# Performance work log

Hardware: AMD Instinct MI355X
Metric: run time of the kernel (lower is better)

The kernel has to match this reference:

```python
import jax, jax.numpy as jnp
import numpy as np

H, KV, D, HID = 36, 4, 128, 4608   # heads, kv heads, head_dim, hidden
THETA = 100000.0
NEG = -1e30


def _rope_neox(pos, x):
    # pos: [T] int, x: [T, nh, D]; neox style: rotate half
    half = D // 2
    inv_freq = 1.0 / (THETA ** (jnp.arange(half, dtype=jnp.float32) / half))
    ang = pos.astype(jnp.float32)[:, None] * inv_freq          # [T, half]
    cos = jnp.cos(ang)[:, None, :]
    sin = jnp.sin(ang)[:, None, :]
    x1, x2 = x[..., :half], x[..., half:]
    return jnp.concatenate([x1 * cos - x2 * sin, x2 * cos + x1 * sin], axis=-1)


def setup_inputs() -> dict:
    key = jax.random.key(0)
    ks = jax.random.split(key, 6)
    T = 2048
    return {
        "positions": jnp.arange(T, dtype=jnp.int32),
        "hidden_states": jax.random.normal(ks[0], (T, HID), dtype=jnp.float32),
        "wqkv": jax.random.normal(ks[1], (H * D + 2 * KV * D, HID), dtype=jnp.float32) * 0.02,
        "bqkv": jax.random.normal(ks[2], (H * D + 2 * KV * D,), dtype=jnp.float32) * 0.02,
        "wo": jax.random.normal(ks[3], (HID, H * D), dtype=jnp.float32) * 0.02,
        "bo": jax.random.normal(ks[4], (HID,), dtype=jnp.float32) * 0.02,
        "window": 1024,
    }


def reference(positions, hidden_states, wqkv, bqkv, wo, bo, window):
    T = hidden_states.shape[0]
    qkv = hidden_states @ wqkv.T + bqkv                         # [T, 5632]
    q, k, v = jnp.split(qkv, [H * D, H * D + KV * D], axis=-1)
    q = q.reshape(T, H, D)
    k = k.reshape(T, KV, D)
    v = v.reshape(T, KV, D)
    q = _rope_neox(positions, q)
    k = _rope_neox(positions, k)
    # GQA: expand kv heads to query heads
    g = H // KV
    k = jnp.repeat(k, g, axis=1)                                # [T, H, D]
    v = jnp.repeat(v, g, axis=1)
    scale = D ** -0.5
    scores = jnp.einsum('thd,shd->hts', q, k) * scale           # [H, T, T]
    t = jnp.arange(T)
    # causal + sliding window: attend to s in (t - window, t]
    mask = (t[None, :] <= t[:, None]) & (t[None, :] > t[:, None] - window)
    scores = jnp.where(mask[None, :, :], scores, NEG)
    p = jax.nn.softmax(scores, axis=-1)
    attn = jnp.einsum('hts,shd->thd', p, v).reshape(T, H * D)
    return attn @ wo.T + bo
```

## Files before the change

kernel.cpp:

```cpp
#include <hip/hip_runtime.h>
#include <hip/hip_bf16.h>
#include <math.h>


#define T_SEQ   2048
#define HIDDEN  4608
#define NHEAD   36
#define NKVH    4
#define HEADDIM 128
#define GQA_G   9
#define NQKV    5632
#define KOFF    4608
#define VOFF    5120
#define NEG_BIG -1e30f
#define BQ 64
#define BS 32
#define NTILE   64
#define PSTR 40

typedef short    bf16x8 __attribute__((ext_vector_type(8)));
typedef _Float16 f16x8  __attribute__((ext_vector_type(8)));
typedef float    f32x4  __attribute__((ext_vector_type(4)));

__device__ inline bf16x8 pack8(float4 u, float4 v) {
    union { bf16x8 v8; __hip_bfloat162 h[4]; } r;
    r.h[0] = __float22bfloat162_rn(make_float2(u.x, u.y));
    r.h[1] = __float22bfloat162_rn(make_float2(u.z, u.w));
    r.h[2] = __float22bfloat162_rn(make_float2(v.x, v.y));
    r.h[3] = __float22bfloat162_rn(make_float2(v.z, v.w));
    return r.v8;
}

typedef const __attribute__((address_space(1))) int* gas_ptr;
typedef __attribute__((address_space(3))) int*       las_ptr;
__device__ __forceinline__ void gload_lds16(const void* g, void* l) {
    __builtin_amdgcn_global_load_lds((gas_ptr)g, (las_ptr)l, 16, 0, 0);
}

__global__ __launch_bounds__(256)
void cvt_bf16_kernel(const float* __restrict__ in, __hip_bfloat16* __restrict__ out,
                     int n8)
{
    for (int i = blockIdx.x * 256 + threadIdx.x; i < n8; i += gridDim.x * 256) {
        const float4 a = *(const float4*)(in + (size_t)i * 8);
        const float4 b = *(const float4*)(in + (size_t)i * 8 + 4);
        *(bf16x8*)(out + (size_t)i * 8) = pack8(a, b);
    }
}

__global__ __launch_bounds__(256)
void gemm_bf16bt_kernel(const __hip_bfloat16* __restrict__ A,
                        const __hip_bfloat16* __restrict__ B,
                        const float* __restrict__ bias,
                        float* __restrict__ C, int N, int K)
{
    __shared__ short As[2][128 * 32];
    __shared__ short Bs[2][128 * 32];

    const int tid  = threadIdx.x;
    const int lane = tid & 63;
    const int wave = tid >> 6;
    const int row0 = blockIdx.y * 128;
    const int col0 = blockIdx.x * 128;
    const int wr   = (wave >> 1) * 64;
    const int wc   = (wave & 1) * 64;
    const int fr   = lane & 15;
    const int fk   = (lane >> 4) * 8;

    const int srow = lane >> 2;
    const int scol = (lane & 3) * 8;

    const __hip_bfloat16* Ag0 = A + (size_t)(row0 + wave * 32 + srow) * K + scol;
    const __hip_bfloat16* Ag1 = Ag0 + (size_t)16 * K;
    const __hip_bfloat16* Bg0 = B + (size_t)(col0 + wave * 32 + srow) * K + scol;
    const __hip_bfloat16* Bg1 = Bg0 + (size_t)16 * K;

    short* Al0[2] = { &As[0][(wave * 32) * 32],      &As[1][(wave * 32) * 32] };
    short* Al1[2] = { &As[0][(wave * 32 + 16) * 32], &As[1][(wave * 32 + 16) * 32] };
    short* Bl0[2] = { &Bs[0][(wave * 32) * 32],      &Bs[1][(wave * 32) * 32] };
    short* Bl1[2] = { &Bs[0][(wave * 32 + 16) * 32], &Bs[1][(wave * 32 + 16) * 32] };

    f32x4 acc[4][4];
    #pragma unroll
    for (int i = 0; i < 4; ++i)
        #pragma unroll
        for (int j = 0; j < 4; ++j)
            #pragma unroll
            for (int r = 0; r < 4; ++r) acc[i][j][r] = 0.0f;

    gload_lds16(Ag0, Al0[0]);
    gload_lds16(Ag1, Al1[0]);
    gload_lds16(Bg0, Bl0[0]);
    gload_lds16(Bg1, Bl1[0]);
    __syncthreads();
    int cur = 0;

    for (int k0 = 0; k0 < K; k0 += 32) {
        if (k0 + 32 < K) {
            const int kn = k0 + 32;
            const int nb = cur ^ 1;
            gload_lds16(Ag0 + kn, Al0[nb]);
            gload_lds16(Ag1 + kn, Al1[nb]);
            gload_lds16(Bg0 + kn, Bl0[nb]);
            gload_lds16(Bg1 + kn, Bl1[nb]);
        }

        bf16x8 af[4], bfr[4];
        #pragma unroll
        for (int i = 0; i < 4; ++i)
            af[i] = *(const bf16x8*)&As[cur][(wr + i * 16 + fr) * 32 + fk];
        #pragma unroll
        for (int j = 0; j < 4; ++j)
            bfr[j] = *(const bf16x8*)&Bs[cur][(wc + j * 16 + fr) * 32 + fk];

        #pragma unroll
        for (int i = 0; i < 4; ++i)
            #pragma unroll
            for (int j = 0; j < 4; ++j)
                acc[i][j] = __builtin_amdgcn_mfma_f32_16x16x32_bf16(
                    af[i], bfr[j], acc[i][j], 0, 0, 0);

        __syncthreads();
        cur ^= 1;
    }

    const int quad = lane >> 4;
    #pragma unroll
    for (int j = 0; j < 4; ++j) {
        const int col = col0 + wc + j * 16 + fr;
        const float bv = bias[col];
        #pragma unroll
        for (int i = 0; i < 4; ++i) {
            const int rowb = row0 + wr + i * 16 + quad * 4;
            #pragma unroll
            for (int r = 0; r < 4; ++r)
                C[(size_t)(rowb + r) * N + col] = acc[i][j][r] + bv;
        }
    }
}

__global__ __launch_bounds__(256)
void prep_kv_kernel(const int* __restrict__ positions,
                    const float* __restrict__ qkv,
                    _Float16* __restrict__ Kt,
                    _Float16* __restrict__ Vt)
{
    const int tile = blockIdx.x;
    const int kvh  = blockIdx.y;
    const int t    = threadIdx.x;
    const size_t ib = ((size_t)kvh * NTILE + tile) * 4096;

    {
        const int s   = t >> 3;
        const int j8  = (t & 7) * 8;
        const int row = tile * BS + s;
        const float* kp = qkv + (size_t)row * NQKV + KOFF + kvh * HEADDIM;
        float x1[8], x2[8];
        *(float4*)&x1[0] = *(const float4*)(kp + j8);
        *(float4*)&x1[4] = *(const float4*)(kp + j8 + 4);
        *(float4*)&x2[0] = *(const float4*)(kp + 64 + j8);
        *(float4*)&x2[4] = *(const float4*)(kp + 64 + j8 + 4);
        const float pos = (float)positions[row];
        f16x8 H1, H2;
        #pragma unroll
        for (int j = 0; j < 8; ++j) {
            const int d = j8 + j;
            const float inv_freq = __expf(-(float)d * (11.512925465f / 64.0f));
            float sn, cs;
            sincosf(pos * inv_freq, &sn, &cs);
            H1[j] = (_Float16)(x1[j] * cs - x2[j] * sn);
            H2[j] = (_Float16)(x2[j] * cs + x1[j] * sn);
        }
        const int gd1 = (t & 7);
        const int gd2 = gd1 + 8;
        *(f16x8*)&Kt[ib + gd1 * 256 + s * 8] = H1;
        *(f16x8*)&Kt[ib + gd2 * 256 + s * 8] = H2;
    }

    {
        const int q  = t >> 6;
        const int d0 = (t & 63) * 2;
        const float* vp = qkv + (size_t)(tile * BS + q * 8) * NQKV + VOFF
                        + kvh * HEADDIM + d0;
        f16x8 V0, V1;
        #pragma unroll
        for (int j = 0; j < 8; ++j) {
            const float2 vv = *(const float2*)(vp + (size_t)j * NQKV);
            V0[j] = (_Float16)vv.x;
            V1[j] = (_Float16)vv.y;
        }
        *(f16x8*)&Vt[ib + q * 1024 + d0 * 8]       = V0;
        *(f16x8*)&Vt[ib + q * 1024 + (d0 + 1) * 8] = V1;
    }
}

__global__ __launch_bounds__(256)
void attn_kernel(const float* __restrict__ qkv,
                 const int* __restrict__ positions,
                 const _Float16* __restrict__ Kt,
                 const _Float16* __restrict__ Vt,
                 __hip_bfloat16* __restrict__ out,
                 const int* __restrict__ windowp)
{
    __shared__ _Float16 KS[2][4096];
    __shared__ _Float16 VS[2][4096];
    __shared__ _Float16 Ps[4][16 * PSTR];

    const int h    = blockIdx.x;
    const int q0   = (T_SEQ / BQ - 1 - blockIdx.y) * BQ;
    const int kvh  = h / GQA_G;
    const int tid  = threadIdx.x;
    const int lane = tid & 63;
    const int wave = tid >> 6;
    const int l15  = lane & 15;
    const int quad = lane >> 4;
    const int window = *windowp;
    const float scale = 0.088388347648318447f * 1.4426950408889634f;

    f16x8 qf[4];
    {
        const int qrow = q0 + wave * 16 + l15;
        const float* qp = qkv + (size_t)qrow * NQKV + h * HEADDIM + quad * 8;
        float qv[32];
        #pragma unroll
        for (int ks = 0; ks < 4; ++ks) {
            *(float4*)&qv[ks * 8]     = *(const float4*)(qp + ks * 32);
            *(float4*)&qv[ks * 8 + 4] = *(const float4*)(qp + ks * 32 + 4);
        }
        const float pos = (float)positions[qrow];
        #pragma unroll
        for (int p = 0; p < 2; ++p)
            #pragma unroll
            for (int j = 0; j < 8; ++j) {
                const int d = p * 32 + quad * 8 + j;
                const float inv_freq = __expf(-(float)d * (11.512925465f / 64.0f));
                float sn, cs;
                sincosf(pos * inv_freq, &sn, &cs);
                const float x1 = qv[p * 8 + j];
                const float x2 = qv[(p + 2) * 8 + j];
                qv[p * 8 + j]       = x1 * cs - x2 * sn;
                qv[(p + 2) * 8 + j] = x2 * cs + x1 * sn;
            }
        #pragma unroll
        for (int ks = 0; ks < 4; ++ks)
            #pragma unroll
            for (int j = 0; j < 8; ++j)
                qf[ks][j] = (_Float16)(qv[ks * 8 + j] * scale);
    }

    f32x4 o[8];
    #pragma unroll
    for (int c = 0; c < 8; ++c)
        #pragma unroll
        for (int r = 0; r < 4; ++r) o[c][r] = 0.0f;
    float mrun[4], lrun[4];
    #pragma unroll
    for (int r = 0; r < 4; ++r) { mrun[r] = NEG_BIG; lrun[r] = 0.0f; }

    int s_lo = q0 - window + 1;
    if (s_lo < 0) s_lo = 0;
    s_lo &= ~(BS - 1);
    const int tile0  = s_lo >> 5;
    const int ntiles = ((q0 + BQ) - s_lo) >> 5;

    const _Float16* gK = Kt + ((size_t)kvh * NTILE) * 4096;
    const _Float16* gV = Vt + ((size_t)kvh * NTILE) * 4096;

    _Float16* Psw = &Ps[wave][0];

    auto STAGE = [&](int buf, int tile) {
        const size_t toff = (size_t)tile * 4096;
        #pragma unroll
        for (int i = 0; i < 2; ++i) {
            const int off = (wave * 2 + i) * 512;
            gload_lds16(gK + toff + off + lane * 8, &KS[buf][off]);
            gload_lds16(gV + toff + off + lane * 8, &VS[buf][off]);
        }
    };

    STAGE(0, tile0);
    __syncthreads();
    int cur = 0;

    for (int it = 0; it < ntiles; ++it) {
        const int st = s_lo + it * BS;
        if (it + 1 < ntiles) STAGE(cur ^ 1, tile0 + it + 1);

        f32x4 acc0, acc1;
        #pragma unroll
        for (int r = 0; r < 4; ++r) { acc0[r] = 0.0f; acc1[r] = 0.0f; }
        #pragma unroll
        for (int ks = 0; ks < 4; ++ks) {
            const int g = (ks * 4 + quad) * 256;
            const f16x8 b0 = *(const f16x8*)&KS[cur][g + l15 * 8];
            const f16x8 b1 = *(const f16x8*)&KS[cur][g + (16 + l15) * 8];
            acc0 = __builtin_amdgcn_mfma_f32_16x16x32_f16(qf[ks], b0, acc0, 0, 0, 0);
            acc1 = __builtin_amdgcn_mfma_f32_16x16x32_f16(qf[ks], b1, acc1, 0, 0, 0);
        }

        const int qb  = q0 + wave * 16 + quad * 4;
        const int s0g = st + l15;
        const int s1g = st + 16 + l15;
        #pragma unroll
        for (int r = 0; r < 4; ++r) {
            const int q = qb + r;
            const bool v0 = (s0g <= q) && (s0g > q - window);
            const bool v1 = (s1g <= q) && (s1g > q - window);
            float a = v0 ? acc0[r] : NEG_BIG;
            float b = v1 ? acc1[r] : NEG_BIG;
            float mx = fmaxf(a, b);
            mx = fmaxf(mx, __shfl_xor(mx, 1));
            mx = fmaxf(mx, __shfl_xor(mx, 2));
            mx = fmaxf(mx, __shfl_xor(mx, 4));
            mx = fmaxf(mx, __shfl_xor(mx, 8));
            if (__any(mx > mrun[r] + 8.0f)) {
                const float mnew  = fmaxf(mrun[r], mx);
                const float alpha = __builtin_amdgcn_exp2f(mrun[r] - mnew);
                mrun[r] = mnew;
                lrun[r] *= alpha;
                #pragma unroll
                for (int c = 0; c < 8; ++c) o[c][r] *= alpha;
            }
            const float e0 = v0 ? __builtin_amdgcn_exp2f(acc0[r] - mrun[r]) : 0.0f;
            const float e1 = v1 ? __builtin_amdgcn_exp2f(acc1[r] - mrun[r]) : 0.0f;
            const _Float16 p0 = (_Float16)e0;
            const _Float16 p1 = (_Float16)e1;
            Psw[(quad * 4 + r) * PSTR + l15]      = p0;
            Psw[(quad * 4 + r) * PSTR + 16 + l15] = p1;
            float sum = (float)p0 + (float)p1;
            sum += __shfl_xor(sum, 1);
            sum += __shfl_xor(sum, 2);
            sum += __shfl_xor(sum, 4);
            sum += __shfl_xor(sum, 8);
            lrun[r] += sum;
        }

        const f16x8 pa = *(const f16x8*)&Psw[l15 * PSTR + quad * 8];
        #pragma unroll
        for (int c = 0; c < 8; ++c) {
            const f16x8 vb = *(const f16x8*)&VS[cur][quad * 1024 + (16 * c + l15) * 8];
            o[c] = __builtin_amdgcn_mfma_f32_16x16x32_f16(pa, vb, o[c], 0, 0, 0);
        }

        __syncthreads();
        cur ^= 1;
    }

    #pragma unroll
    for (int r = 0; r < 4; ++r) {
        const float inv = 1.0f / lrun[r];
        __hip_bfloat16* op = out
                  + (size_t)(q0 + wave * 16 + quad * 4 + r) * (NHEAD * HEADDIM)
                  + h * HEADDIM + l15;
        #pragma unroll
        for (int c = 0; c < 8; ++c) op[16 * c] = __float2bfloat16(o[c][r] * inv);
    }
}

extern "C" void kernel_launch(void* const* d_in, const int* in_sizes, int n_in,
                              void* d_out, int out_size, void* d_ws, size_t ws_size,
                              hipStream_t stream)
{
    const int*   positions = (const int*)d_in[0];
    const float* hidden    = (const float*)d_in[1];
    const float* wqkv      = (const float*)d_in[2];
    const float* bqkv      = (const float*)d_in[3];
    const float* wo        = (const float*)d_in[4];
    const float* bo        = (const float*)d_in[5];
    const int*   windowp   = (const int*)d_in[6];
    float* outp = (float*)d_out;

    float* qkv = (float*)d_ws;
    __hip_bfloat16* hbf  = (__hip_bfloat16*)(qkv + (size_t)T_SEQ * NQKV);
    __hip_bfloat16* wqbf = hbf  + (size_t)T_SEQ * HIDDEN;
    __hip_bfloat16* wobf = wqbf + (size_t)NQKV * HIDDEN;
    __hip_bfloat16* abf  = wobf + (size_t)HIDDEN * HIDDEN;
    _Float16*       Kt   = (_Float16*)(abf + (size_t)T_SEQ * HIDDEN);
    _Float16*       Vt   = Kt + (size_t)NKVH * NTILE * 4096;

    cvt_bf16_kernel<<<1024, 256, 0, stream>>>(hidden, hbf, T_SEQ * HIDDEN / 8);
    cvt_bf16_kernel<<<2048, 256, 0, stream>>>(wqkv, wqbf, NQKV * HIDDEN / 8);
    cvt_bf16_kernel<<<2048, 256, 0, stream>>>(wo, wobf, HIDDEN * HIDDEN / 8);

    gemm_bf16bt_kernel<<<dim3(NQKV / 128, T_SEQ / 128), 256, 0, stream>>>(
        hbf, wqbf, bqkv, qkv, NQKV, HIDDEN);

    prep_kv_kernel<<<dim3(NTILE, NKVH), 256, 0, stream>>>(
        positions, qkv, Kt, Vt);

    attn_kernel<<<dim3(NHEAD, T_SEQ / BQ), 256, 0, stream>>>(
        qkv, positions, Kt, Vt, abf, windowp);

    gemm_bf16bt_kernel<<<dim3(HIDDEN / 128, T_SEQ / 128), 256, 0, stream>>>(
        abf, wobf, bo, outp, HIDDEN, HIDDEN);
}
```

Baseline: 627.3 us.

## Transpose attention MFMAs so each lane owns one query row's softmax

```diff
diff --git a/kernel.cpp b/kernel.cpp
--- a/kernel.cpp
+++ b/kernel.cpp
@@ -20,6 +20,7 @@
 
 typedef short    bf16x8 __attribute__((ext_vector_type(8)));
 typedef _Float16 f16x8  __attribute__((ext_vector_type(8)));
+typedef _Float16 f16x4  __attribute__((ext_vector_type(4)));
 typedef float    f32x4  __attribute__((ext_vector_type(4)));
 
 __device__ inline bf16x8 pack8(float4 u, float4 v) {
@@ -218,16 +219,16 @@
     const float scale = 0.088388347648318447f * 1.4426950408889634f;
 
     f16x8 qf[4];
+    const int q_g = q0 + wave * 16 + l15;
     {
-        const int qrow = q0 + wave * 16 + l15;
-        const float* qp = qkv + (size_t)qrow * NQKV + h * HEADDIM + quad * 8;
+        const float* qp = qkv + (size_t)q_g * NQKV + h * HEADDIM + quad * 8;
         float qv[32];
         #pragma unroll
         for (int ks = 0; ks < 4; ++ks) {
             *(float4*)&qv[ks * 8]     = *(const float4*)(qp + ks * 32);
             *(float4*)&qv[ks * 8 + 4] = *(const float4*)(qp + ks * 32 + 4);
         }
-        const float pos = (float)positions[qrow];
+        const float pos = (float)positions[q_g];
         #pragma unroll
         for (int p = 0; p < 2; ++p)
             #pragma unroll
@@ -253,9 +254,8 @@
     for (int c = 0; c < 8; ++c)
         #pragma unroll
         for (int r = 0; r < 4; ++r) o[c][r] = 0.0f;
-    float mrun[4], lrun[4];
-    #pragma unroll
-    for (int r = 0; r < 4; ++r) { mrun[r] = NEG_BIG; lrun[r] = 0.0f; }
+    float mrun = -1e9f;
+    float lrun = 0.0f;
 
     int s_lo = q0 - window + 1;
     if (s_lo < 0) s_lo = 0;
@@ -294,66 +294,74 @@
             const int g = (ks * 4 + quad) * 256;
             const f16x8 b0 = *(const f16x8*)&KS[cur][g + l15 * 8];
             const f16x8 b1 = *(const f16x8*)&KS[cur][g + (16 + l15) * 8];
-            acc0 = __builtin_amdgcn_mfma_f32_16x16x32_f16(qf[ks], b0, acc0, 0, 0, 0);
-            acc1 = __builtin_amdgcn_mfma_f32_16x16x32_f16(qf[ks], b1, acc1, 0, 0, 0);
-        }
-
-        const int qb  = q0 + wave * 16 + quad * 4;
-        const int s0g = st + l15;
-        const int s1g = st + 16 + l15;
+            acc0 = __builtin_amdgcn_mfma_f32_16x16x32_f16(b0, qf[ks], acc0, 0, 0, 0);
+            acc1 = __builtin_amdgcn_mfma_f32_16x16x32_f16(b1, qf[ks], acc1, 0, 0, 0);
+        }
+
+        const int dq = q_g - st;
+        float sv[8];
         #pragma unroll
         for (int r = 0; r < 4; ++r) {
-            const int q = qb + r;
-            const bool v0 = (s0g <= q) && (s0g > q - window);
-            const bool v1 = (s1g <= q) && (s1g > q - window);
-            float a = v0 ? acc0[r] : NEG_BIG;
-            float b = v1 ? acc1[r] : NEG_BIG;
-            float mx = fmaxf(a, b);
-            mx = fmaxf(mx, __shfl_xor(mx, 1));
-            mx = fmaxf(mx, __shfl_xor(mx, 2));
-            mx = fmaxf(mx, __shfl_xor(mx, 4));
-            mx = fmaxf(mx, __shfl_xor(mx, 8));
-            if (__any(mx > mrun[r] + 8.0f)) {
-                const float mnew  = fmaxf(mrun[r], mx);
-                const float alpha = __builtin_amdgcn_exp2f(mrun[r] - mnew);
-                mrun[r] = mnew;
-                lrun[r] *= alpha;
+            const int o0 = quad * 4 + r;
+            const bool v0 = (unsigned)(dq - o0)      < (unsigned)window;
+            const bool v1 = (unsigned)(dq - o0 - 16) < (unsigned)window;
+            sv[r]     = v0 ? acc0[r] : -2e9f;
+            sv[4 + r] = v1 ? acc1[r] : -2e9f;
+        }
+        float mx = sv[0];
+        #pragma unroll
+        for (int i = 1; i < 8; ++i) mx = fmaxf(mx, sv[i]);
+        mx = fmaxf(mx, __shfl_xor(mx, 16));
+        mx = fmaxf(mx, __shfl_xor(mx, 32));
+        if (__any(mx > mrun + 8.0f)) {
+            const float mnew  = fmaxf(mrun, mx);
+            const float alpha = __builtin_amdgcn_exp2f(mrun - mnew);
+            mrun = mnew;
+            lrun *= alpha;
+            #pragma unroll
+            for (int c = 0; c < 8; ++c)
                 #pragma unroll
-                for (int c = 0; c < 8; ++c) o[c][r] *= alpha;
-            }
-            const float e0 = v0 ? __builtin_amdgcn_exp2f(acc0[r] - mrun[r]) : 0.0f;
-            const float e1 = v1 ? __builtin_amdgcn_exp2f(acc1[r] - mrun[r]) : 0.0f;
-            const _Float16 p0 = (_Float16)e0;
-            const _Float16 p1 = (_Float16)e1;
-            Psw[(quad * 4 + r) * PSTR + l15]      = p0;
-            Psw[(quad * 4 + r) * PSTR + 16 + l15] = p1;
-            float sum = (float)p0 + (float)p1;
-            sum += __shfl_xor(sum, 1);
-            sum += __shfl_xor(sum, 2);
-            sum += __shfl_xor(sum, 4);
-            sum += __shfl_xor(sum, 8);
-            lrun[r] += sum;
-        }
-
+                for (int r = 0; r < 4; ++r) o[c][r] *= alpha;
+        }
+        float e[8];
+        float sum = 0.0f;
+        #pragma unroll
+        for (int i = 0; i < 8; ++i) {
+            e[i] = __builtin_amdgcn_exp2f(sv[i] - mrun);
+            sum += e[i];
+        }
+        sum += __shfl_xor(sum, 16);
+        sum += __shfl_xor(sum, 32);
+        lrun += sum;
+
+        f16x4 pl, ph;
+        #pragma unroll
+        for (int r = 0; r < 4; ++r) { pl[r] = (_Float16)e[r]; ph[r] = (_Float16)e[4 + r]; }
+        *(f16x4*)&Psw[l15 * PSTR + quad * 4]      = pl;
+        *(f16x4*)&Psw[l15 * PSTR + 16 + quad * 4] = ph;
         const f16x8 pa = *(const f16x8*)&Psw[l15 * PSTR + quad * 8];
+
         #pragma unroll
         for (int c = 0; c < 8; ++c) {
             const f16x8 vb = *(const f16x8*)&VS[cur][quad * 1024 + (16 * c + l15) * 8];
-            o[c] = __builtin_amdgcn_mfma_f32_16x16x32_f16(pa, vb, o[c], 0, 0, 0);
+            o[c] = __builtin_amdgcn_mfma_f32_16x16x32_f16(vb, pa, o[c], 0, 0, 0);
         }
 
         __syncthreads();
         cur ^= 1;
     }
 
-    #pragma unroll
-    for (int r = 0; r < 4; ++r) {
-        const float inv = 1.0f / lrun[r];
-        __hip_bfloat16* op = out
-                  + (size_t)(q0 + wave * 16 + quad * 4 + r) * (NHEAD * HEADDIM)
-                  + h * HEADDIM + l15;
-        #pragma unroll
-        for (int c = 0; c < 8; ++c) op[16 * c] = __float2bfloat16(o[c][r] * inv);
+    {
+        const float inv = 1.0f / lrun;
+        __hip_bfloat16* op = out + (size_t)q_g * (NHEAD * HEADDIM)
+                           + h * HEADDIM + quad * 4;
+        #pragma unroll
+        for (int c = 0; c < 8; ++c) {
+            union { ushort4 u; __hip_bfloat16 x[4]; } w;
+            #pragma unroll
+            for (int r = 0; r < 4; ++r) w.x[r] = __float2bfloat16(o[c][r] * inv);
+            *(ushort4*)&op[16 * c] = w.u;
+        }
     }
 }
 
```

New measurement: 576.8 us. 8.0% less time.
